# Performance work log

Hardware: AMD Instinct MI355X
Metric: run time of the kernel (lower is better)

The kernel has to match this reference:

```python
import jax, jax.numpy as jnp
import numpy as np

B, T, H, K = 16, 2048, 512, 15
FIRE_TH = 1.0
SMOOTH = 1.0
NOISE_TH = 0.0
LN_EPS = 1e-5


def setup_inputs() -> dict:
    key = jax.random.key(0)
    ks = jax.random.split(key, 8)
    s = lambda n: 1.0 / np.sqrt(n)
    return {
        "x": jax.random.normal(ks[0], (B, T, H), jnp.float32),
        "x_lens": jax.random.randint(ks[1], (B,), T // 2, T + 1),
        "pw1_w": jax.random.normal(ks[2], (2 * H, H), jnp.float32) * s(H),
        "pw1_b": jnp.zeros((2 * H,), jnp.float32),
        "dw_w": jax.random.normal(ks[3], (H, K), jnp.float32) * s(K),
        "dw_b": jnp.zeros((H,), jnp.float32),
        "ln_g": jnp.ones((H,), jnp.float32),
        "ln_b": jnp.zeros((H,), jnp.float32),
        "pw2_w": jax.random.normal(ks[4], (H, H), jnp.float32) * s(H),
        "pw2_b": jnp.zeros((H,), jnp.float32),
        "lin_w": jax.random.normal(ks[5], (H,), jnp.float32) * s(H),
        "lin_b": jnp.zeros((), jnp.float32),
    }


def _layer_norm(x, g, b):
    m = x.mean(-1, keepdims=True)
    v = ((x - m) ** 2).mean(-1, keepdims=True)
    return (x - m) * jax.lax.rsqrt(v + LN_EPS) * g + b


def _swish(x):
    return x * jax.nn.sigmoid(x)


def _conv_module(x, pw1_w, pw1_b, dw_w, dw_b, ln_g, ln_b, pw2_w, pw2_b):
    # wenet ConvolutionModule (causal, layer_norm): pw-conv -> GLU -> causal depthwise -> LN -> swish -> pw-conv
    h = jnp.einsum('bth,oh->bto', x, pw1_w) + pw1_b          # (B,T,2H)
    h = h[..., :H] * jax.nn.sigmoid(h[..., H:])              # GLU over channel halves
    hp = jnp.pad(h, ((0, 0), (K - 1, 0), (0, 0)))            # causal left pad
    rhs = dw_w.T[:, None, :]                                 # (K, 1, H) depthwise kernel
    h = jax.lax.conv_general_dilated(
        hp, rhs, window_strides=(1,), padding='VALID',
        dimension_numbers=('NWC', 'WIO', 'NWC'),
        feature_group_count=H) + dw_b                        # (B,T,H)
    h = _swish(_layer_norm(h, ln_g, ln_b))
    return jnp.einsum('bth,oh->bto', h, pw2_w) + pw2_b


def _cif_scan(x, alphas):
    # sequential integrate-and-fire over time, batched over B
    def step(carry, inp):
        integrate, frame = carry
        alpha, xt = inp                                       # (B,), (B,H)
        dist = FIRE_TH - integrate
        integrate = integrate + alpha
        fire = integrate >= FIRE_TH
        cur = jnp.where(fire, dist, alpha)
        remain = alpha - cur
        frame_acc = frame + cur[:, None] * xt
        new_frame = jnp.where(fire[:, None], remain[:, None] * xt, frame_acc)
        new_int = jnp.where(fire, integrate - FIRE_TH, integrate)
        return (new_int, new_frame), (integrate, frame_acc)
    init = (jnp.zeros((B,), x.dtype), jnp.zeros((B, H), x.dtype))
    _, (fires, frames) = jax.lax.scan(step, init, (alphas.T, x.transpose(1, 0, 2)))
    return fires.T, frames.transpose(1, 0, 2)                 # (B,T), (B,T,H)


def _gather_fired(fires, frames):
    # ragged gather of fired frames into a fixed (B,T,H) padded buffer
    mask = fires >= FIRE_TH                                   # (B,T)
    dest = jnp.where(mask, jnp.cumsum(mask, axis=1) - 1, T)   # dump non-fired to slot T
    out = jnp.zeros((B, T + 1, H), frames.dtype)
    out = out.at[jnp.arange(B)[:, None], dest].set(frames)
    fired = out[:, :T]
    return fired, jnp.flip(fired, axis=-1)                    # torch.flip(dims=[1]) flips hidden dim


def reference(x, x_lens, pw1_w, pw1_b, dw_w, dw_b, ln_g, ln_b, pw2_w, pw2_b, lin_w, lin_b):
    mask = (jnp.arange(T)[None, :] < x_lens[:, None]).astype(x.dtype)   # (B,T)
    hidden = _conv_module(x, pw1_w, pw1_b, dw_w, dw_b, ln_g, ln_b, pw2_w, pw2_b)
    logits = jnp.einsum('bth,h->bt', hidden, lin_w) + lin_b
    alphas = jax.nn.relu(jax.nn.sigmoid(logits) * SMOOTH - NOISE_TH) * mask
    predicted_token_nums = alphas.sum(-1)
    fires, frames = _cif_scan(x, alphas)
    fired_frames, r_fired_frames = _gather_fired(fires, frames)
    return fired_frames, predicted_token_nums, r_fired_frames
```

## Files before the change

### kernel.cpp

```cpp
#include <hip/hip_runtime.h>
#include <math.h>

#define B_ 16
#define T_ 2048
#define H_ 512
#define K_ 15
#define M_ (B_*T_)

typedef __attribute__((ext_vector_type(8))) short short8;
typedef __attribute__((ext_vector_type(4))) float f32x4;

__device__ __forceinline__ unsigned short f2bf(float f) {
  union { float f; unsigned u; } v; v.f = f;
  unsigned r = v.u + 0x7FFFu + ((v.u >> 16) & 1u);
  return (unsigned short)(r >> 16);
}
__device__ __forceinline__ float bf2f(unsigned short b) {
  union { float f; unsigned u; } v; v.u = ((unsigned)b) << 16;
  return v.f;
}

__device__ __forceinline__ void async_load16(const void* g, void* l) {
  __builtin_amdgcn_global_load_lds((const __attribute__((address_space(1))) void*)g,
                                   (__attribute__((address_space(3))) void*)l, 16, 0, 0);
}

__global__ void convx_k(const float* __restrict__ x, unsigned short* __restrict__ hi,
                        unsigned short* __restrict__ lo, int n4) {
  int i = blockIdx.x * blockDim.x + threadIdx.x;
  int stride = gridDim.x * blockDim.x;
  for (; i < n4; i += stride) {
    float4 v = ((const float4*)x)[i];
    ushort4 h, l;
    h.x = f2bf(v.x); l.x = f2bf(v.x - bf2f(h.x));
    h.y = f2bf(v.y); l.y = f2bf(v.y - bf2f(h.y));
    h.z = f2bf(v.z); l.z = f2bf(v.z - bf2f(h.z));
    h.w = f2bf(v.w); l.w = f2bf(v.w - bf2f(h.w));
    ((ushort4*)hi)[i] = h;
    ((ushort4*)lo)[i] = l;
  }
}

__global__ __launch_bounds__(256) void weff_k(const float* __restrict__ pw2_w,
    const float* __restrict__ pw2_b, const float* __restrict__ lin_w,
    const float* __restrict__ lin_b, float* __restrict__ weff) {
  __shared__ float red[256];
  if (blockIdx.x < 8) {
    int h = blockIdx.x * 64 + (threadIdx.x & 63);
    int og = threadIdx.x >> 6;
    float acc = 0.f;
    for (int o = og * 128; o < og * 128 + 128; ++o) acc += pw2_w[o * H_ + h] * lin_w[o];
    red[threadIdx.x] = acc;
    __syncthreads();
    if (threadIdx.x < 64)
      weff[h] = red[threadIdx.x] + red[threadIdx.x + 64] + red[threadIdx.x + 128] + red[threadIdx.x + 192];
  } else {
    int i = threadIdx.x;
    red[i] = pw2_b[i] * lin_w[i] + pw2_b[i + 256] * lin_w[i + 256];
    __syncthreads();
    for (int s = 128; s > 0; s >>= 1) {
      if (i < s) red[i] += red[i + s];
      __syncthreads();
    }
    if (i == 0) weff[H_] = red[0] + lin_b[0];
  }
}

__global__ __launch_bounds__(256) void gemm_mfma_k(
    const unsigned short* __restrict__ Ahi, const unsigned short* __restrict__ Alo,
    const unsigned short* __restrict__ Whi, const unsigned short* __restrict__ Wlo,
    const float* __restrict__ bias, float* __restrict__ g) {
  __shared__ short Ah[2][128 * 32];
  __shared__ short Al[2][128 * 32];
  __shared__ short Bh[2][128 * 32];
  __shared__ short Bl[2][128 * 32];
  const int tid = threadIdx.x;
  const int bid = blockIdx.x;
  const int xcd = bid & 7, ii = bid >> 3;
  const int m0 = (((xcd << 5) + (ii >> 3))) * 128;
  const int n0 = (ii & 7) * 64;
  const int w = tid >> 6, lane = tid & 63;
  const int wr = w >> 1, wc = w & 1;

  f32x4 acc[4][4];
#pragma unroll
  for (int mt = 0; mt < 4; ++mt)
#pragma unroll
    for (int nt = 0; nt < 4; ++nt) acc[mt][nt] = (f32x4){0.f, 0.f, 0.f, 0.f};

  int offA[2], offB[2], ldsb[2];
#pragma unroll
  for (int j = 0; j < 2; ++j) {
    int L = j * 256 + tid;
    int r = L >> 2;
    int csrc = (L & 3) ^ ((r >> 1) & 3);
    offA[j] = (m0 + r) * 512 + csrc * 8;
    int wrow = (r < 64) ? (n0 + r) : (n0 + 448 + r);
    offB[j] = wrow * 512 + csrc * 8;
    ldsb[j] = __builtin_amdgcn_readfirstlane((j * 256 + w * 64) * 16);
  }

  const int q = lane >> 4;
  int aAddr[4], bAddr[4];
#pragma unroll
  for (int mt = 0; mt < 4; ++mt) {
    int rA = wr * 64 + mt * 16 + (lane & 15);
    aAddr[mt] = rA * 64 + (q ^ ((rA >> 1) & 3)) * 16;
  }
#pragma unroll
  for (int nt = 0; nt < 4; ++nt) {
    int rB = (nt >> 1) * 64 + wc * 32 + (nt & 1) * 16 + (lane & 15);
    bAddr[nt] = rB * 64 + (q ^ ((rB >> 1) & 3)) * 16;
  }

#pragma unroll
  for (int j = 0; j < 2; ++j) {
    async_load16(Ahi + offA[j], (char*)Ah[0] + ldsb[j]);
    async_load16(Alo + offA[j], (char*)Al[0] + ldsb[j]);
  }
#pragma unroll
  for (int j = 0; j < 2; ++j) {
    async_load16(Whi + offB[j], (char*)Bh[0] + ldsb[j]);
    async_load16(Wlo + offB[j], (char*)Bl[0] + ldsb[j]);
  }

  short8 ah[4], al[4], bh[4], bl[4];

#pragma unroll 2
  for (int kk = 0; kk < 15; ++kk) {
    const int cur = kk & 1;
    const int nxt = cur ^ 1;
    const int k1 = (kk + 1) * 32;

    __builtin_amdgcn_sched_barrier(0);
    asm volatile("s_waitcnt vmcnt(4)" ::: "memory");
    __builtin_amdgcn_s_barrier();
    __builtin_amdgcn_sched_barrier(0);
#pragma unroll
    for (int mt = 0; mt < 4; ++mt) {
      ah[mt] = *(const short8*)((const char*)Ah[cur] + aAddr[mt]);
      al[mt] = *(const short8*)((const char*)Al[cur] + aAddr[mt]);
    }
#pragma unroll
    for (int j = 0; j < 2; ++j) {
      async_load16(Ahi + offA[j] + k1, (char*)Ah[nxt] + ldsb[j]);
      async_load16(Alo + offA[j] + k1, (char*)Al[nxt] + ldsb[j]);
    }

    __builtin_amdgcn_sched_barrier(0);
    asm volatile("s_waitcnt vmcnt(4)" ::: "memory");
    __builtin_amdgcn_s_barrier();
    __builtin_amdgcn_sched_barrier(0);
#pragma unroll
    for (int nt = 0; nt < 4; ++nt) {
      bh[nt] = *(const short8*)((const char*)Bh[cur] + bAddr[nt]);
      bl[nt] = *(const short8*)((const char*)Bl[cur] + bAddr[nt]);
    }
#pragma unroll
    for (int j = 0; j < 2; ++j) {
      async_load16(Whi + offB[j] + k1, (char*)Bh[nxt] + ldsb[j]);
      async_load16(Wlo + offB[j] + k1, (char*)Bl[nxt] + ldsb[j]);
    }

    __builtin_amdgcn_s_setprio(1);
#pragma unroll
    for (int mt = 0; mt < 4; ++mt)
#pragma unroll
      for (int nt = 0; nt < 4; ++nt) {
        acc[mt][nt] = __builtin_amdgcn_mfma_f32_16x16x32_bf16(ah[mt], bh[nt], acc[mt][nt], 0, 0, 0);
        acc[mt][nt] = __builtin_amdgcn_mfma_f32_16x16x32_bf16(al[mt], bh[nt], acc[mt][nt], 0, 0, 0);
        acc[mt][nt] = __builtin_amdgcn_mfma_f32_16x16x32_bf16(ah[mt], bl[nt], acc[mt][nt], 0, 0, 0);
      }
    __builtin_amdgcn_s_setprio(0);
  }

  {
    __builtin_amdgcn_sched_barrier(0);
    asm volatile("s_waitcnt vmcnt(4)" ::: "memory");
    __builtin_amdgcn_s_barrier();
    __builtin_amdgcn_sched_barrier(0);
#pragma unroll
    for (int mt = 0; mt < 4; ++mt) {
      ah[mt] = *(const short8*)((const char*)Ah[1] + aAddr[mt]);
      al[mt] = *(const short8*)((const char*)Al[1] + aAddr[mt]);
    }
    __builtin_amdgcn_sched_barrier(0);
    asm volatile("s_waitcnt vmcnt(0)" ::: "memory");
    __builtin_amdgcn_s_barrier();
    __builtin_amdgcn_sched_barrier(0);
#pragma unroll
    for (int nt = 0; nt < 4; ++nt) {
      bh[nt] = *(const short8*)((const char*)Bh[1] + bAddr[nt]);
      bl[nt] = *(const short8*)((const char*)Bl[1] + bAddr[nt]);
    }
    __builtin_amdgcn_s_setprio(1);
#pragma unroll
    for (int mt = 0; mt < 4; ++mt)
#pragma unroll
      for (int nt = 0; nt < 4; ++nt) {
        acc[mt][nt] = __builtin_amdgcn_mfma_f32_16x16x32_bf16(ah[mt], bh[nt], acc[mt][nt], 0, 0, 0);
        acc[mt][nt] = __builtin_amdgcn_mfma_f32_16x16x32_bf16(al[mt], bh[nt], acc[mt][nt], 0, 0, 0);
        acc[mt][nt] = __builtin_amdgcn_mfma_f32_16x16x32_bf16(ah[mt], bl[nt], acc[mt][nt], 0, 0, 0);
      }
    __builtin_amdgcn_s_setprio(0);
  }

  const int col = lane & 15, rq = lane >> 4;
#pragma unroll
  for (int mt = 0; mt < 4; ++mt) {
#pragma unroll
    for (int ntp = 0; ntp < 2; ++ntp) {
      int gcol = n0 + wc * 32 + ntp * 16 + col;
      float ba = bias[gcol];
      float bg = bias[512 + gcol];
#pragma unroll
      for (int r = 0; r < 4; ++r) {
        int m = m0 + wr * 64 + mt * 16 + rq * 4 + r;
        float a = acc[mt][ntp][r] + ba;
        float gt = acc[mt][2 + ntp][r] + bg;
        g[(size_t)m * 512 + gcol] = a / (1.f + expf(-gt));
      }
    }
  }
}

__global__ __launch_bounds__(512) void conv_ln_k(const float* __restrict__ g,
    const float* __restrict__ dw_w, const float* __restrict__ dw_b,
    const float* __restrict__ ln_g, const float* __restrict__ ln_b,
    const float* __restrict__ weff, const int* __restrict__ x_lens,
    float* __restrict__ aT) {
  __shared__ float wlds[H_ * K_];
  __shared__ float tbuf[16][512];
  __shared__ float mvs[16], rss[16];
  const int tid = threadIdx.x;
  const int c = tid;
  const int t0 = blockIdx.x * 64;
  const int b = blockIdx.y;

  for (int i = tid; i < H_ * K_; i += 512) wlds[i] = dw_w[i];
  const int xlen = x_lens[b];
  const float* gb = g + ((size_t)b * T_) * H_ + c;

  float gwin[30];
#pragma unroll
  for (int i = 0; i < 30; ++i) {
    int t = t0 - 14 + i;
    gwin[i] = (t >= 0) ? gb[(size_t)t * H_] : 0.f;
  }
  __syncthreads();
  float wreg[15];
#pragma unroll
  for (int k = 0; k < 15; ++k) wreg[k] = wlds[c * 15 + k];
  const float dwb = dw_b[c], lg = ln_g[c], lb = ln_b[c], we = weff[c];
  const float beff = weff[H_];
  const int tt = tid >> 5, p = tid & 31;

#pragma unroll 1
  for (int qc = 0; qc < 4; ++qc) {
    float h2[16];
#pragma unroll
    for (int j = 0; j < 16; ++j) {
      float s = dwb;
#pragma unroll
      for (int k = 0; k < 15; ++k) s += gwin[j + k] * wreg[k];
      h2[j] = s;
      tbuf[j][c] = s;
    }
    __syncthreads();
    float s1 = 0.f, s2 = 0.f;
#pragma unroll
    for (int k = 0; k < 16; ++k) {
      float v = tbuf[tt][k * 32 + p];
      s1 += v; s2 += v * v;
    }
#pragma unroll
    for (int off = 16; off > 0; off >>= 1) {
      s1 += __shfl_down(s1, off, 32);
      s2 += __shfl_down(s2, off, 32);
    }
    if (p == 0) {
      float m = s1 * (1.f / 512.f);
      float v = s2 * (1.f / 512.f) - m * m;
      mvs[tt] = m;
      rss[tt] = rsqrtf(v + 1e-5f);
    }
    __syncthreads();
#pragma unroll
    for (int j = 0; j < 16; ++j) {
      float y = (h2[j] - mvs[j]) * rss[j] * lg + lb;
      float sw = y / (1.f + expf(-y));
      tbuf[j][c] = sw * we;
    }
    __syncthreads();
    float s = 0.f;
#pragma unroll
    for (int k = 0; k < 16; ++k) s += tbuf[tt][k * 32 + p];
#pragma unroll
    for (int off = 16; off > 0; off >>= 1) s += __shfl_down(s, off, 32);
    if (p == 0) {
      float logit = s + beff;
      float a = 1.f / (1.f + expf(-logit));
      int t = t0 + qc * 16 + tt;
      if (t >= xlen) a = 0.f;
      aT[t * B_ + b] = a;
    }
    if (qc < 3) {
#pragma unroll
      for (int i = 0; i < 14; ++i) gwin[i] = gwin[i + 16];
#pragma unroll
      for (int i = 0; i < 16; ++i)
        gwin[14 + i] = gb[(size_t)(t0 + qc * 16 + 16 + i) * H_];
    }
    __syncthreads();
  }
}

__global__ __launch_bounds__(64) void cif_p1_k(const float* __restrict__ aT,
                                               float* __restrict__ chk) {
  const int b = threadIdx.x;
  if (b >= B_) return;
  const float* ar = aT + b;
  float integ = 0.f;
  float bufA[32], bufB[32];
#pragma unroll
  for (int j = 0; j < 32; ++j) bufA[j] = ar[j * B_];
#pragma unroll 1
  for (int s = 0; s < 64; s += 2) {
#pragma unroll
    for (int j = 0; j < 32; ++j) bufB[j] = ar[((s + 1) * 32 + j) * B_];
    chk[s * B_ + b] = integ;
#pragma unroll
    for (int j = 0; j < 32; ++j) {
      float ni = integ + bufA[j];
      integ = ni - floorf(ni);
    }
    if (s + 2 < 64) {
#pragma unroll
      for (int j = 0; j < 32; ++j) bufA[j] = ar[((s + 2) * 32 + j) * B_];
    }
    chk[(s + 1) * B_ + b] = integ;
#pragma unroll
    for (int j = 0; j < 32; ++j) {
      float ni = integ + bufB[j];
      integ = ni - floorf(ni);
    }
  }
}

__global__ __launch_bounds__(64) void cif_p2_k(const float* __restrict__ aT,
    const float* __restrict__ chk, float* __restrict__ wdT, float* __restrict__ wrT,
    int* __restrict__ fire_pos, int* __restrict__ nfires, float* __restrict__ tok) {
  const int b = blockIdx.x;
  const int seg = threadIdx.x;
  const int t0 = seg * 32;
  float integ = chk[seg * B_ + b];
  float a[32];
#pragma unroll
  for (int j = 0; j < 32; ++j) a[j] = aT[(t0 + j) * B_ + b];
  unsigned fmask = 0u;
  float ssum = 0.f;
#pragma unroll
  for (int j = 0; j < 32; ++j) {
    float al = a[j];
    float dist = 1.0f - integ;
    float ni = integ + al;
    bool fire = ni >= 1.0f;
    float cur = fire ? dist : al;
    wdT[(t0 + j) * B_ + b] = cur;
    wrT[(t0 + j) * B_ + b] = al - cur;
    if (fire) fmask |= (1u << j);
    integ = ni - floorf(ni);
    ssum += al;
  }
  const int cnt = __popc(fmask);
  int incl = cnt;
#pragma unroll
  for (int off = 1; off < 64; off <<= 1) {
    int v = __shfl_up(incl, off, 64);
    if (seg >= off) incl += v;
  }
  int idx = incl - cnt;
  unsigned m = fmask;
  while (m) {
    int j = __ffs(m) - 1;
    m &= m - 1;
    fire_pos[b * T_ + idx++] = t0 + j;
  }
  if (seg == 63) nfires[b] = incl;
#pragma unroll
  for (int off = 32; off > 0; off >>= 1) ssum += __shfl_down(ssum, off, 64);
  if (seg == 0) tok[b] = ssum;
}

__global__ __launch_bounds__(128) void frames_k(const float* __restrict__ x,
    const float* __restrict__ aT, const float* __restrict__ wdT,
    const float* __restrict__ wrT, const int* __restrict__ fire_pos,
    const int* __restrict__ nfires, float* __restrict__ out0, float* __restrict__ out2) {
  const int b = blockIdx.y;
  const int j = blockIdx.x;
  const int h = threadIdx.x << 2;
  const size_t ob = ((size_t)b * T_ + j) * H_;
  if (j >= nfires[b]) {
    float4 z = make_float4(0.f, 0.f, 0.f, 0.f);
    *(float4*)(out0 + ob + h) = z;
    *(float4*)(out2 + ob + h) = z;
    return;
  }
  const int te = fire_pos[b * T_ + j];
  const int ts = (j > 0) ? fire_pos[b * T_ + j - 1] : -1;
  const float* xb = x + ((size_t)b * T_) * H_;
  float4 acc = make_float4(0.f, 0.f, 0.f, 0.f);
  if (j > 0) {
    float w = wrT[ts * B_ + b];
    float4 xv = *(const float4*)(xb + (size_t)ts * H_ + h);
    acc.x = w * xv.x; acc.y = w * xv.y; acc.z = w * xv.z; acc.w = w * xv.w;
  }
  for (int t = ts + 1; t < te; ++t) {
    float w = aT[t * B_ + b];
    float4 xv = *(const float4*)(xb + (size_t)t * H_ + h);
    acc.x += w * xv.x; acc.y += w * xv.y; acc.z += w * xv.z; acc.w += w * xv.w;
  }
  {
    float w = wdT[te * B_ + b];
    float4 xv = *(const float4*)(xb + (size_t)te * H_ + h);
    acc.x += w * xv.x; acc.y += w * xv.y; acc.z += w * xv.z; acc.w += w * xv.w;
  }
  *(float4*)(out0 + ob + h) = acc;
  float4 racc = make_float4(acc.w, acc.z, acc.y, acc.x);
  *(float4*)(out2 + ob + (H_ - 4 - h)) = racc;
}

extern "C" void kernel_launch(void* const* d_in, const int* in_sizes, int n_in,
                              void* d_out, int out_size, void* d_ws, size_t ws_size,
                              hipStream_t stream) {
  const float* x     = (const float*)d_in[0];
  const int*   xlens = (const int*)d_in[1];
  const float* pw1_w = (const float*)d_in[2];
  const float* pw1_b = (const float*)d_in[3];
  const float* dw_w  = (const float*)d_in[4];
  const float* dw_b  = (const float*)d_in[5];
  const float* ln_g  = (const float*)d_in[6];
  const float* ln_b  = (const float*)d_in[7];
  const float* pw2_w = (const float*)d_in[8];
  const float* pw2_b = (const float*)d_in[9];
  const float* lin_w = (const float*)d_in[10];
  const float* lin_b = (const float*)d_in[11];

  float* out0 = (float*)d_out;
  float* tok  = out0 + (size_t)B_ * T_ * H_;
  float* out2 = tok + B_;

  char* ws = (char*)d_ws;
  float* g             = (float*)ws;
  unsigned short* Ahi  = (unsigned short*)(ws + (size_t)M_ * H_ * 4);
  unsigned short* Alo  = Ahi + (size_t)M_ * H_;
  unsigned short* Whi  = Alo + (size_t)M_ * H_;
  unsigned short* Wlo  = Whi + (size_t)2 * H_ * H_;
  float* aT       = (float*)(Wlo + (size_t)2 * H_ * H_);
  float* wdT      = aT + B_ * T_;
  float* wrT      = wdT + B_ * T_;
  int*   fire_pos = (int*)(wrT + B_ * T_);
  int*   nfires   = fire_pos + B_ * T_;
  float* weff     = (float*)(nfires + 64);
  float* chk      = weff + 1024;

  convx_k<<<2048, 256, 0, stream>>>(x, Ahi, Alo, M_ * H_ / 4);
  convx_k<<<256, 256, 0, stream>>>(pw1_w, Whi, Wlo, 2 * H_ * H_ / 4);
  weff_k<<<9, 256, 0, stream>>>(pw2_w, pw2_b, lin_w, lin_b, weff);
  gemm_mfma_k<<<2048, 256, 0, stream>>>(Ahi, Alo, Whi, Wlo, pw1_b, g);
  conv_ln_k<<<dim3(32, 16), 512, 0, stream>>>(g, dw_w, dw_b, ln_g, ln_b, weff, xlens, aT);
  cif_p1_k<<<1, 64, 0, stream>>>(aT, chk);
  cif_p2_k<<<16, 64, 0, stream>>>(aT, chk, wdT, wrT, fire_pos, nfires, tok);
  frames_k<<<dim3(2048, 16), 128, 0, stream>>>(x, aT, wdT, wrT, fire_pos, nfires, out0, out2);
}
```

Measured before the change: 442.8 us.

## Fuse CIF scan phases into one kernel and batch frames per block

Merges the two CIF kernels into one per-batch kernel. It stages alphas in LDS and has one lane compute the segment checkpoints serially, which removes a launch and the global chk round trip. The frames kernel now handles 16 fired frames per block and carries the previous fire position forward, cutting block count and repeated fire_pos loads. The fp32-to-bf16 split kernel now processes 8 elements per thread with 16-byte stores. Risks include the serial single-lane scan per block, and fewer blocks in frames_k giving less parallelism for long segments.

```diff
diff --git a/kernel.cpp b/kernel.cpp
--- a/kernel.cpp
+++ b/kernel.cpp
@@ -8,6 +8,7 @@
 #define M_ (B_*T_)
 
 typedef __attribute__((ext_vector_type(8))) short short8;
+typedef __attribute__((ext_vector_type(8))) unsigned short ushort8;
 typedef __attribute__((ext_vector_type(4))) float f32x4;
 
 __device__ __forceinline__ unsigned short f2bf(float f) {
@@ -26,18 +27,23 @@
 }
 
 __global__ void convx_k(const float* __restrict__ x, unsigned short* __restrict__ hi,
-                        unsigned short* __restrict__ lo, int n4) {
+                        unsigned short* __restrict__ lo, int n8) {
   int i = blockIdx.x * blockDim.x + threadIdx.x;
   int stride = gridDim.x * blockDim.x;
-  for (; i < n4; i += stride) {
-    float4 v = ((const float4*)x)[i];
-    ushort4 h, l;
-    h.x = f2bf(v.x); l.x = f2bf(v.x - bf2f(h.x));
-    h.y = f2bf(v.y); l.y = f2bf(v.y - bf2f(h.y));
-    h.z = f2bf(v.z); l.z = f2bf(v.z - bf2f(h.z));
-    h.w = f2bf(v.w); l.w = f2bf(v.w - bf2f(h.w));
-    ((ushort4*)hi)[i] = h;
-    ((ushort4*)lo)[i] = l;
+  for (; i < n8; i += stride) {
+    float4 v0 = ((const float4*)x)[2 * i];
+    float4 v1 = ((const float4*)x)[2 * i + 1];
+    ushort8 h, l;
+    h[0] = f2bf(v0.x); l[0] = f2bf(v0.x - bf2f(h[0]));
+    h[1] = f2bf(v0.y); l[1] = f2bf(v0.y - bf2f(h[1]));
+    h[2] = f2bf(v0.z); l[2] = f2bf(v0.z - bf2f(h[2]));
+    h[3] = f2bf(v0.w); l[3] = f2bf(v0.w - bf2f(h[3]));
+    h[4] = f2bf(v1.x); l[4] = f2bf(v1.x - bf2f(h[4]));
+    h[5] = f2bf(v1.y); l[5] = f2bf(v1.y - bf2f(h[5]));
+    h[6] = f2bf(v1.z); l[6] = f2bf(v1.z - bf2f(h[6]));
+    h[7] = f2bf(v1.w); l[7] = f2bf(v1.w - bf2f(h[7]));
+    ((ushort8*)hi)[i] = h;
+    ((ushort8*)lo)[i] = l;
   }
 }
 
@@ -315,48 +321,36 @@
   }
 }
 
-__global__ __launch_bounds__(64) void cif_p1_k(const float* __restrict__ aT,
-                                               float* __restrict__ chk) {
-  const int b = threadIdx.x;
-  if (b >= B_) return;
-  const float* ar = aT + b;
-  float integ = 0.f;
-  float bufA[32], bufB[32];
-#pragma unroll
-  for (int j = 0; j < 32; ++j) bufA[j] = ar[j * B_];
-#pragma unroll 1
-  for (int s = 0; s < 64; s += 2) {
-#pragma unroll
-    for (int j = 0; j < 32; ++j) bufB[j] = ar[((s + 1) * 32 + j) * B_];
-    chk[s * B_ + b] = integ;
-#pragma unroll
-    for (int j = 0; j < 32; ++j) {
-      float ni = integ + bufA[j];
-      integ = ni - floorf(ni);
-    }
-    if (s + 2 < 64) {
-#pragma unroll
-      for (int j = 0; j < 32; ++j) bufA[j] = ar[((s + 2) * 32 + j) * B_];
-    }
-    chk[(s + 1) * B_ + b] = integ;
-#pragma unroll
-    for (int j = 0; j < 32; ++j) {
-      float ni = integ + bufB[j];
-      integ = ni - floorf(ni);
-    }
-  }
-}
-
-__global__ __launch_bounds__(64) void cif_p2_k(const float* __restrict__ aT,
-    const float* __restrict__ chk, float* __restrict__ wdT, float* __restrict__ wrT,
+__global__ __launch_bounds__(64) void cif_k(const float* __restrict__ aT,
+    float* __restrict__ wdT, float* __restrict__ wrT,
     int* __restrict__ fire_pos, int* __restrict__ nfires, float* __restrict__ tok) {
+  __shared__ float alds[T_];
+  __shared__ float chks[64];
   const int b = blockIdx.x;
   const int seg = threadIdx.x;
+
+  for (int t = seg; t < T_; t += 64) alds[t] = aT[t * B_ + b];
+  __syncthreads();
+
+  if (seg == 0) {
+    float integ = 0.f;
+#pragma unroll 1
+    for (int s = 0; s < 64; ++s) {
+      chks[s] = integ;
+#pragma unroll
+      for (int j = 0; j < 32; ++j) {
+        float ni = integ + alds[s * 32 + j];
+        integ = ni - floorf(ni);
+      }
+    }
+  }
+  __syncthreads();
+
   const int t0 = seg * 32;
-  float integ = chk[seg * B_ + b];
+  float integ = chks[seg];
   float a[32];
 #pragma unroll
-  for (int j = 0; j < 32; ++j) a[j] = aT[(t0 + j) * B_ + b];
+  for (int j = 0; j < 32; ++j) a[j] = alds[t0 + j];
   unsigned fmask = 0u;
   float ssum = 0.f;
 #pragma unroll
@@ -392,42 +386,49 @@
   if (seg == 0) tok[b] = ssum;
 }
 
+#define JCHUNK 16
 __global__ __launch_bounds__(128) void frames_k(const float* __restrict__ x,
     const float* __restrict__ aT, const float* __restrict__ wdT,
     const float* __restrict__ wrT, const int* __restrict__ fire_pos,
     const int* __restrict__ nfires, float* __restrict__ out0, float* __restrict__ out2) {
   const int b = blockIdx.y;
-  const int j = blockIdx.x;
+  const int j0 = blockIdx.x * JCHUNK;
   const int h = threadIdx.x << 2;
-  const size_t ob = ((size_t)b * T_ + j) * H_;
-  if (j >= nfires[b]) {
-    float4 z = make_float4(0.f, 0.f, 0.f, 0.f);
-    *(float4*)(out0 + ob + h) = z;
-    *(float4*)(out2 + ob + h) = z;
-    return;
-  }
-  const int te = fire_pos[b * T_ + j];
-  const int ts = (j > 0) ? fire_pos[b * T_ + j - 1] : -1;
+  const int nf = nfires[b];
   const float* xb = x + ((size_t)b * T_) * H_;
-  float4 acc = make_float4(0.f, 0.f, 0.f, 0.f);
-  if (j > 0) {
-    float w = wrT[ts * B_ + b];
-    float4 xv = *(const float4*)(xb + (size_t)ts * H_ + h);
-    acc.x = w * xv.x; acc.y = w * xv.y; acc.z = w * xv.z; acc.w = w * xv.w;
-  }
-  for (int t = ts + 1; t < te; ++t) {
-    float w = aT[t * B_ + b];
-    float4 xv = *(const float4*)(xb + (size_t)t * H_ + h);
-    acc.x += w * xv.x; acc.y += w * xv.y; acc.z += w * xv.z; acc.w += w * xv.w;
-  }
-  {
-    float w = wdT[te * B_ + b];
-    float4 xv = *(const float4*)(xb + (size_t)te * H_ + h);
-    acc.x += w * xv.x; acc.y += w * xv.y; acc.z += w * xv.z; acc.w += w * xv.w;
-  }
-  *(float4*)(out0 + ob + h) = acc;
-  float4 racc = make_float4(acc.w, acc.z, acc.y, acc.x);
-  *(float4*)(out2 + ob + (H_ - 4 - h)) = racc;
+  int ts = (j0 > 0) ? fire_pos[b * T_ + j0 - 1] : -1;
+
+#pragma unroll 1
+  for (int j = j0; j < j0 + JCHUNK; ++j) {
+    const size_t ob = ((size_t)b * T_ + j) * H_;
+    if (j >= nf) {
+      float4 z = make_float4(0.f, 0.f, 0.f, 0.f);
+      *(float4*)(out0 + ob + h) = z;
+      *(float4*)(out2 + ob + h) = z;
+      continue;
+    }
+    const int te = fire_pos[b * T_ + j];
+    float4 acc = make_float4(0.f, 0.f, 0.f, 0.f);
+    if (j > 0) {
+      float wv = wrT[ts * B_ + b];
+      float4 xv = *(const float4*)(xb + (size_t)ts * H_ + h);
+      acc.x = wv * xv.x; acc.y = wv * xv.y; acc.z = wv * xv.z; acc.w = wv * xv.w;
+    }
+    for (int t = ts + 1; t < te; ++t) {
+      float wv = aT[t * B_ + b];
+      float4 xv = *(const float4*)(xb + (size_t)t * H_ + h);
+      acc.x += wv * xv.x; acc.y += wv * xv.y; acc.z += wv * xv.z; acc.w += wv * xv.w;
+    }
+    {
+      float wv = wdT[te * B_ + b];
+      float4 xv = *(const float4*)(xb + (size_t)te * H_ + h);
+      acc.x += wv * xv.x; acc.y += wv * xv.y; acc.z += wv * xv.z; acc.w += wv * xv.w;
+    }
+    *(float4*)(out0 + ob + h) = acc;
+    float4 racc = make_float4(acc.w, acc.z, acc.y, acc.x);
+    *(float4*)(out2 + ob + (H_ - 4 - h)) = racc;
+    ts = te;
+  }
 }
 
 extern "C" void kernel_launch(void* const* d_in, const int* in_sizes, int n_in,
@@ -462,14 +463,12 @@
   int*   fire_pos = (int*)(wrT + B_ * T_);
   int*   nfires   = fire_pos + B_ * T_;
   float* weff     = (float*)(nfires + 64);
-  float* chk      = weff + 1024;
-
-  convx_k<<<2048, 256, 0, stream>>>(x, Ahi, Alo, M_ * H_ / 4);
-  convx_k<<<256, 256, 0, stream>>>(pw1_w, Whi, Wlo, 2 * H_ * H_ / 4);
+
+  convx_k<<<2048, 256, 0, stream>>>(x, Ahi, Alo, M_ * H_ / 8);
+  convx_k<<<256, 256, 0, stream>>>(pw1_w, Whi, Wlo, 2 * H_ * H_ / 8);
   weff_k<<<9, 256, 0, stream>>>(pw2_w, pw2_b, lin_w, lin_b, weff);
   gemm_mfma_k<<<2048, 256, 0, stream>>>(Ahi, Alo, Whi, Wlo, pw1_b, g);
   conv_ln_k<<<dim3(32, 16), 512, 0, stream>>>(g, dw_w, dw_b, ln_g, ln_b, weff, xlens, aT);
-  cif_p1_k<<<1, 64, 0, stream>>>(aT, chk);
-  cif_p2_k<<<16, 64, 0, stream>>>(aT, chk, wdT, wrT, fire_pos, nfires, tok);
-  frames_k<<<dim3(2048, 16), 128, 0, stream>>>(x, aT, wdT, wrT, fire_pos, nfires, out0, out2);
-}
+  cif_k<<<16, 64, 0, stream>>>(aT, wdT, wrT, fire_pos, nfires, tok);
+  frames_k<<<dim3(T_ / JCHUNK, 16), 128, 0, stream>>>(x, aT, wdT, wrT, fire_pos, nfires, out0, out2);
+}
```

Result: slower. 459.0 us (+3.6%).
